# Kernel tuning notes

Measured on AMD Instinct MI355X. Metric: run time of the kernel, lower is better.

Reference implementation:

```python
import jax, jax.numpy as jnp
import numpy as np

N_HEADS = 16


def setup_inputs() -> dict:
    key = jax.random.key(0)
    k0, k1, k2 = jax.random.split(key, 3)
    B, S, D = 8, 1024, 1024
    x = jax.random.normal(k0, (B, S, D), dtype=jnp.float32)
    W_qkv = jax.random.normal(k1, (D, 3 * D), dtype=jnp.float32) * 0.02
    b_qkv = jnp.zeros((3 * D,), dtype=jnp.float32)
    W_proj = jax.random.normal(k2, (D, D), dtype=jnp.float32) * 0.02
    b_proj = jnp.zeros((D,), dtype=jnp.float32)
    return {"x": x, "W_qkv": W_qkv, "b_qkv": b_qkv, "W_proj": W_proj, "b_proj": b_proj}


def reference(x, W_qkv, b_qkv, W_proj, b_proj):
    B, S, D = x.shape
    H = N_HEADS
    hd = D // H
    scale = hd ** (-0.5)
    # qkv projection: (B,S,3D) -> (3,B,H,S,hd)
    qkv = x @ W_qkv + b_qkv
    qkv = qkv.reshape(B, S, 3, H, hd).transpose(2, 0, 3, 1, 4)
    q, k, v = qkv[0], qkv[1], qkv[2]
    # explicit materialized attention scores (B,H,S,S), softmax over keys
    scores = jnp.einsum("bhqd,bhkd->bhqk", q, k) * scale
    attn = jax.nn.softmax(scores, axis=-1)
    # weighted values -> concat heads -> output projection
    out = jnp.einsum("bhqk,bhkd->bhqd", attn, v)
    out = out.transpose(0, 2, 1, 3).reshape(B, S, D)
    return out @ W_proj + b_proj
```

## Files before the change

### kernel.cpp

```cpp
#include <hip/hip_runtime.h>
#include <hip/hip_bf16.h>

typedef __bf16 bf16_t;
typedef __attribute__((ext_vector_type(8))) __bf16 bf16x8;
typedef __attribute__((ext_vector_type(4))) float f32x4;
typedef __attribute__((ext_vector_type(16))) float f32x16;

#define QSCALE 0.18033688011112042f
#define RESCALE_THR 11.5f

#define OFF_XB      ((size_t)0)
#define OFF_WQKVT   ((size_t)16777216)
#define OFF_WPROJT  ((size_t)(16777216 + 6291456))
#define OFF_Q       ((size_t)(16777216 + 6291456 + 2097152))
#define OFF_K       (OFF_Q + (size_t)16777216)
#define OFF_V       (OFF_K + (size_t)16777216)
#define OFF_O       OFF_XB

typedef const __attribute__((address_space(1))) void* as1cv;
typedef __attribute__((address_space(3))) void* as3v;

__device__ __forceinline__ void load_lds16(const void* g, void* l) {
  __builtin_amdgcn_global_load_lds((as1cv)g, (as3v)l, 16, 0, 0);
}

__device__ __forceinline__ f32x4 mfma16(bf16x8 a, bf16x8 b, f32x4 c) {
  return __builtin_amdgcn_mfma_f32_16x16x32_bf16(a, b, c, 0, 0, 0);
}
__device__ __forceinline__ f32x16 mfma32(bf16x8 a, bf16x8 b, f32x16 c) {
  return __builtin_amdgcn_mfma_f32_32x32x16_bf16(a, b, c, 0, 0, 0);
}

__device__ __forceinline__ float fexp2(float x) { return __builtin_amdgcn_exp2f(x); }

__device__ __forceinline__ unsigned pack2bf(float a, float b) {
  union { bf16_t h[2]; unsigned u; } x;
  x.h[0] = (bf16_t)a; x.h[1] = (bf16_t)b;
  return x.u;
}

__device__ __forceinline__ bf16x8 frag_from_words(unsigned w0, unsigned w1,
                                                  unsigned w2, unsigned w3) {
  union { unsigned u[4]; bf16x8 v; } x;
  x.u[0] = w0; x.u[1] = w1; x.u[2] = w2; x.u[3] = w3;
  return x.v;
}

__device__ __forceinline__ bf16x8 ldsr(const bf16_t* lds, int row, int slotbyte) {
  return *(const bf16x8*)((const char*)lds + row * 128 +
                          (slotbyte ^ ((row & 7) << 4)));
}


__global__ __launch_bounds__(256) void cvt_bf16_kernel(
    const float* __restrict__ in, bf16_t* __restrict__ out, int n8) {
  int i = blockIdx.x * blockDim.x + threadIdx.x;
  if (i >= n8) return;
  const float4* p = (const float4*)in + (size_t)i * 2;
  float4 a = p[0], b = p[1];
  bf16x8 o;
  o[0] = (bf16_t)a.x; o[1] = (bf16_t)a.y; o[2] = (bf16_t)a.z; o[3] = (bf16_t)a.w;
  o[4] = (bf16_t)b.x; o[5] = (bf16_t)b.y; o[6] = (bf16_t)b.z; o[7] = (bf16_t)b.w;
  ((bf16x8*)out)[i] = o;
}

__global__ __launch_bounds__(256) void transpose_cvt(
    const float* __restrict__ W, bf16_t* __restrict__ Wt, int rows, int cols) {
  __shared__ float t[32][33];
  const int c0 = blockIdx.x * 32, r0 = blockIdx.y * 32;
  const int tx = threadIdx.x, ty = threadIdx.y;
  for (int rr = ty; rr < 32; rr += 8)
    t[rr][tx] = W[(size_t)(r0 + rr) * cols + c0 + tx];
  __syncthreads();
  for (int rr = ty; rr < 32; rr += 8)
    Wt[(size_t)(c0 + rr) * rows + r0 + tx] = (bf16_t)t[tx][rr];
}


__device__ __forceinline__ void gemm_mainloop_1024(
    const bf16_t* __restrict__ A, const bf16_t* __restrict__ Bt,
    int m0, int n0, bf16_t* Alds, bf16_t* Blds, f32x4 acc[4][4]) {
  const int tid = threadIdx.x;
  const int w = tid >> 6, lane = tid & 63;
  const int wr = w >> 1, wc = w & 1;
  const int lr = lane & 15, lg = lane >> 4;
#pragma unroll
  for (int m = 0; m < 4; ++m)
#pragma unroll
    for (int n = 0; n < 4; ++n)
      acc[m][n] = f32x4{0.f, 0.f, 0.f, 0.f};

  const int crow = lane >> 3;
  const int cels = (((lane & 7) ^ crow) * 8);
  const int rx = (lr & 7) << 4;

  for (int kt = 0; kt < 16; ++kt) {
    const int k0 = kt * 64;
#pragma unroll
    for (int it = 0; it < 4; ++it) {
      const int c = it * 4 + w;
      const int rA = c * 8 + crow;
      load_lds16(A + (size_t)(m0 + rA) * 1024 + k0 + cels, (char*)Alds + c * 1024);
      load_lds16(Bt + (size_t)(n0 + rA) * 1024 + k0 + cels, (char*)Blds + c * 1024);
    }
    asm volatile("s_waitcnt vmcnt(0)" ::: "memory");
    __syncthreads();

    bf16x8 af[4][2], bfr[4][2];
#pragma unroll
    for (int m = 0; m < 4; ++m)
#pragma unroll
      for (int kk = 0; kk < 2; ++kk)
        af[m][kk] = *(const bf16x8*)((const char*)Alds + (wr * 64 + m * 16 + lr) * 128 +
                                     ((kk * 64 + lg * 16) ^ rx));
#pragma unroll
    for (int n = 0; n < 4; ++n)
#pragma unroll
      for (int kk = 0; kk < 2; ++kk)
        bfr[n][kk] = *(const bf16x8*)((const char*)Blds + (wc * 64 + n * 16 + lr) * 128 +
                                      ((kk * 64 + lg * 16) ^ rx));
#pragma unroll
    for (int kk = 0; kk < 2; ++kk)
#pragma unroll
      for (int m = 0; m < 4; ++m)
#pragma unroll
        for (int n = 0; n < 4; ++n)
          acc[m][n] = mfma16(af[m][kk], bfr[n][kk], acc[m][n]);
    __syncthreads();
  }
}

__device__ __forceinline__ void xcd_remap(int bid, int MT_PER, int* mt, int* nt) {
  const int r = bid & 7, q = bid >> 3;
  *mt = r * MT_PER + (q & (MT_PER - 1));
  *nt = q / MT_PER;
}


__global__ __launch_bounds__(256) void gemm_qkv(
    const bf16_t* __restrict__ A, const bf16_t* __restrict__ Bt,
    const float* __restrict__ bias,
    bf16_t* __restrict__ Qh, bf16_t* __restrict__ Kh, bf16_t* __restrict__ Vt) {
  __shared__ alignas(128) bf16_t Alds[128 * 64];
  __shared__ alignas(128) bf16_t Blds[128 * 64];
  int mt, nt;
  xcd_remap(blockIdx.x, 8, &mt, &nt);
  const int m0 = mt * 128, n0 = nt * 128;
  f32x4 acc[4][4];
  gemm_mainloop_1024(A, Bt, m0, n0, Alds, Blds, acc);

  const int tid = threadIdx.x, w = tid >> 6, lane = tid & 63;
  const int wr = w >> 1, wc = w & 1, lr = lane & 15, lg = lane >> 4;
  const int section = n0 >> 10;
#pragma unroll
  for (int n = 0; n < 4; ++n) {
    const int c = n0 + wc * 64 + n * 16 + lr;
    const float bi = bias[c];
    const int d1024 = c & 1023;
    const int h = d1024 >> 6, d = d1024 & 63;
#pragma unroll
    for (int m = 0; m < 4; ++m) {
#pragma unroll
      for (int j = 0; j < 4; ++j) {
        const int r = m0 + wr * 64 + m * 16 + lg * 4 + j;
        const int b = r >> 10, s = r & 1023;
        const size_t hb = ((size_t)(b * 16 + h)) << 16;
        const float v = acc[m][n][j] + bi;
        if (section == 0)      Qh[hb + (size_t)s * 64 + d] = (bf16_t)(v * QSCALE);
        else if (section == 1) Kh[hb + (size_t)s * 64 + d] = (bf16_t)v;
        else                   Vt[hb + (size_t)d * 1024 + s] = (bf16_t)v;
      }
    }
  }
}


__global__ __launch_bounds__(256) void gemm_out(
    const bf16_t* __restrict__ A, const bf16_t* __restrict__ Bt,
    const float* __restrict__ bias, float* __restrict__ out) {
  __shared__ alignas(128) bf16_t Alds[128 * 64];
  __shared__ alignas(128) bf16_t Blds[128 * 64];
  int mt, nt;
  xcd_remap(blockIdx.x, 8, &mt, &nt);
  const int m0 = mt * 128, n0 = nt * 128;
  f32x4 acc[4][4];
  gemm_mainloop_1024(A, Bt, m0, n0, Alds, Blds, acc);

  const int tid = threadIdx.x, w = tid >> 6, lane = tid & 63;
  const int wr = w >> 1, wc = w & 1, lr = lane & 15, lg = lane >> 4;
#pragma unroll
  for (int n = 0; n < 4; ++n) {
    const int c = n0 + wc * 64 + n * 16 + lr;
    const float bi = bias[c];
#pragma unroll
    for (int m = 0; m < 4; ++m)
#pragma unroll
      for (int j = 0; j < 4; ++j) {
        const int r = m0 + wr * 64 + m * 16 + lg * 4 + j;
        out[(size_t)r * 1024 + c] = acc[m][n][j] + bi;
      }
  }
}


__global__ __launch_bounds__(256, 4) void attn_kernel(
    const bf16_t* __restrict__ Qh, const bf16_t* __restrict__ Kh,
    const bf16_t* __restrict__ Vt, bf16_t* __restrict__ Ob) {
  __shared__ alignas(128) bf16_t Klds[2][64 * 64];
  __shared__ alignas(128) bf16_t Vlds[2][64 * 64];

  const int x = blockIdx.x;
  const int bh = ((x & 7) << 4) | (x >> 6);
  const int qt = (x >> 3) & 7;
  const int b = bh >> 4, h = bh & 15;
  const int tid = threadIdx.x, w = tid >> 6, lane = tid & 63;
  const int q31 = lane & 31, hi = lane >> 5;
  const size_t base = (size_t)bh << 16;

  const int qrow0 = qt * 128 + w * 32;

  bf16x8 qf[4];
#pragma unroll
  for (int c = 0; c < 4; ++c)
    qf[c] = *(const bf16x8*)(Qh + base + (size_t)(qrow0 + q31) * 64 + hi * 8 + 16 * c);

  f32x16 oacc0, oacc1;
#pragma unroll
  for (int r = 0; r < 16; ++r) { oacc0[r] = 0.f; oacc1[r] = 0.f; }
  float mreg = -1e30f, lreg = 0.f;

  const int srow = lane >> 3;
  const int sslot = (((lane & 7) ^ srow) << 3);

#define STAGE_KV(bsel, kt_)                                                        \
  do {                                                                             \
    _Pragma("unroll")                                                              \
    for (int it = 0; it < 2; ++it) {                                               \
      const int c = it * 4 + w;                                                    \
      const int r = c * 8 + srow;                                                  \
      load_lds16(Kh + base + (size_t)((kt_) * 64 + r) * 64 + sslot,                \
                 (char*)&Klds[bsel][0] + c * 1024);                                \
      load_lds16(Vt + base + (size_t)r * 1024 + (kt_) * 64 + sslot,                \
                 (char*)&Vlds[bsel][0] + c * 1024);                                \
    }                                                                              \
  } while (0)

  STAGE_KV(0, 0);
  asm volatile("s_waitcnt vmcnt(0)" ::: "memory");
  __syncthreads();
  int cur = 0;

  for (int kt = 0; kt < 16; ++kt) {
    if (kt + 1 < 16) STAGE_KV(cur ^ 1, kt + 1);

    const bf16_t* Kb = &Klds[cur][0];
    const bf16_t* Vb = &Vlds[cur][0];

    f32x16 st0, st1;
#pragma unroll
    for (int r = 0; r < 16; ++r) { st0[r] = 0.f; st1[r] = 0.f; }
#pragma unroll
    for (int c = 0; c < 4; ++c) {
      const int sb = hi * 16 + 32 * c;
      bf16x8 k0 = ldsr(Kb, q31, sb);
      bf16x8 k1 = ldsr(Kb, 32 + q31, sb);
      __builtin_amdgcn_s_setprio(1);
      st0 = mfma32(k0, qf[c], st0);
      st1 = mfma32(k1, qf[c], st1);
      __builtin_amdgcn_s_setprio(0);
    }

    float mx[8];
#pragma unroll
    for (int r = 0; r < 8; ++r)
      mx[r] = fmaxf(fmaxf(st0[r], st0[r + 8]), fmaxf(st1[r], st1[r + 8]));
#pragma unroll
    for (int r = 0; r < 4; ++r) mx[r] = fmaxf(mx[r], mx[r + 4]);
    float tm = fmaxf(fmaxf(mx[0], mx[1]), fmaxf(mx[2], mx[3]));
    tm = fmaxf(tm, __shfl_xor(tm, 32));

    if (!__all(tm - mreg <= RESCALE_THR)) {
      const float mnew = fmaxf(mreg, tm);
      const float corr = fexp2(mreg - mnew);
      lreg *= corr;
#pragma unroll
      for (int r = 0; r < 16; ++r) { oacc0[r] *= corr; oacc1[r] *= corr; }
      mreg = mnew;
    }

    bf16x8 pa[4];
    float psum = 0.f;
#define GROUP(KC, STV, BASE)                                                   \
    {                                                                          \
      const float e0 = fexp2(STV[BASE + 0] - mreg);                            \
      const float e1 = fexp2(STV[BASE + 1] - mreg);                            \
      const float e2 = fexp2(STV[BASE + 2] - mreg);                            \
      const float e3 = fexp2(STV[BASE + 3] - mreg);                            \
      const float e4 = fexp2(STV[BASE + 4] - mreg);                            \
      const float e5 = fexp2(STV[BASE + 5] - mreg);                            \
      const float e6 = fexp2(STV[BASE + 6] - mreg);                            \
      const float e7 = fexp2(STV[BASE + 7] - mreg);                            \
      psum += ((e0 + e1) + (e2 + e3)) + ((e4 + e5) + (e6 + e7));               \
      unsigned wa = pack2bf(e0, e1), wb = pack2bf(e4, e5);                     \
      asm volatile("v_permlane32_swap_b32 %0, %1" : "+v"(wa), "+v"(wb));       \
      unsigned wc = pack2bf(e2, e3), wd = pack2bf(e6, e7);                     \
      asm volatile("v_permlane32_swap_b32 %0, %1" : "+v"(wc), "+v"(wd));       \
      pa[KC] = frag_from_words(wa, wc, wb, wd);                                \
    }
    GROUP(0, st0, 0)
    GROUP(1, st0, 8)
    GROUP(2, st1, 0)
    GROUP(3, st1, 8)
#undef GROUP
    lreg += psum + __shfl_xor(psum, 32);

#pragma unroll
    for (int kc = 0; kc < 4; ++kc) {
      const int sb = hi * 16 + 32 * kc;
      bf16x8 v0 = ldsr(Vb, q31, sb);
      bf16x8 v1 = ldsr(Vb, 32 + q31, sb);
      __builtin_amdgcn_s_setprio(1);
      oacc0 = mfma32(v0, pa[kc], oacc0);
      oacc1 = mfma32(v1, pa[kc], oacc1);
      __builtin_amdgcn_s_setprio(0);
    }

    asm volatile("s_waitcnt vmcnt(0)" ::: "memory");
    __syncthreads();
    cur ^= 1;
  }
#undef STAGE_KV

  const float inv = 1.0f / lreg;
  const int s_tok = qrow0 + q31;
  bf16_t* obase = Ob + (size_t)(b * 1024 + s_tok) * 1024 + h * 64;
#pragma unroll
  for (int i = 0; i < 8; ++i) {
    const int dbase = ((2 * i) & 3) + 8 * ((2 * i) >> 2) + 4 * hi;
    *(unsigned*)(obase + dbase) =
        pack2bf(oacc0[2 * i] * inv, oacc0[2 * i + 1] * inv);
    *(unsigned*)(obase + 32 + dbase) =
        pack2bf(oacc1[2 * i] * inv, oacc1[2 * i + 1] * inv);
  }
}


extern "C" void kernel_launch(void* const* d_in, const int* in_sizes, int n_in,
                              void* d_out, int out_size, void* d_ws, size_t ws_size,
                              hipStream_t stream) {
  const float* x     = (const float*)d_in[0];
  const float* Wqkv  = (const float*)d_in[1];
  const float* bqkv  = (const float*)d_in[2];
  const float* Wproj = (const float*)d_in[3];
  const float* bproj = (const float*)d_in[4];
  float* out = (float*)d_out;
  char* ws = (char*)d_ws;

  bf16_t* Xb  = (bf16_t*)(ws + OFF_XB);
  bf16_t* Wqt = (bf16_t*)(ws + OFF_WQKVT);
  bf16_t* Wpt = (bf16_t*)(ws + OFF_WPROJT);
  bf16_t* Qh  = (bf16_t*)(ws + OFF_Q);
  bf16_t* Kh  = (bf16_t*)(ws + OFF_K);
  bf16_t* Vt  = (bf16_t*)(ws + OFF_V);
  bf16_t* Ob  = (bf16_t*)(ws + OFF_O);

  cvt_bf16_kernel<<<4096, 256, 0, stream>>>(x, Xb, 1048576);
  transpose_cvt<<<dim3(96, 32), dim3(32, 8), 0, stream>>>(Wqkv, Wqt, 1024, 3072);
  transpose_cvt<<<dim3(32, 32), dim3(32, 8), 0, stream>>>(Wproj, Wpt, 1024, 1024);
  gemm_qkv<<<1536, 256, 0, stream>>>(Xb, Wqt, bqkv, Qh, Kh, Vt);
  attn_kernel<<<1024, 256, 0, stream>>>(Qh, Kh, Vt, Ob);
  gemm_out<<<512, 256, 0, stream>>>(Ob, Wpt, bproj, out);
}
```

Measured before the change: 179.4 us.

## Rewrite QKV GEMM with 256x256 tiles, 8 waves and double-buffered LDS pipeline

Replaces the 128x128 QKV projection GEMM with a 512-thread, 256x256-tile kernel. It double-buffers A and B in LDS and interleaves global-to-LDS staging of the next K slice with MFMA phases, using raw s_barrier and s_setprio. The larger tile raises arithmetic intensity and cuts the block count from 1536 to 384. In exchange it uses 128KB of LDS and many more accumulator registers, so occupancy is lower, and it relies on hand-placed waitcnt and barrier ordering for correctness.

```diff
diff --git a/kernel.cpp b/kernel.cpp
--- a/kernel.cpp
+++ b/kernel.cpp
@@ -46,7 +46,7 @@
   return x.v;
 }
 
-__device__ __forceinline__ bf16x8 ldsr(const bf16_t* lds, int row, int slotbyte) {
+__device__ __forceinline__ bf16x8 ldsr(const void* lds, int row, int slotbyte) {
   return *(const bf16x8*)((const char*)lds + row * 128 +
                           (slotbyte ^ ((row & 7) << 4)));
 }
@@ -76,6 +76,153 @@
     Wt[(size_t)(c0 + rr) * rows + r0 + tx] = (bf16_t)t[tx][rr];
 }
 
+#define GBAR asm volatile("s_barrier" ::: "memory")
+
+
+__global__ __launch_bounds__(512, 2) void gemm_qkv(
+    const bf16_t* __restrict__ A, const bf16_t* __restrict__ Bt,
+    const float* __restrict__ bias,
+    bf16_t* __restrict__ Qh, bf16_t* __restrict__ Kh, bf16_t* __restrict__ Vt) {
+  __shared__ alignas(128) char Alds[2 * 32768];
+  __shared__ alignas(128) char Blds[2 * 32768];
+
+  const int rx8 = blockIdx.x & 7, q = blockIdx.x >> 3;
+  const int mt = rx8 * 4 + (q & 3), nt = q >> 2;
+  const int m0 = mt * 256, n0 = nt * 256;
+
+  const int tid = threadIdx.x;
+  const int w = tid >> 6, lane = tid & 63;
+  const int wr = w >> 2, wc = w & 3;
+  const int lr = lane & 15, lg = lane >> 4;
+
+  f32x4 acc[8][4];
+#pragma unroll
+  for (int m = 0; m < 8; ++m)
+#pragma unroll
+    for (int n = 0; n < 4; ++n)
+      acc[m][n] = f32x4{0.f, 0.f, 0.f, 0.f};
+
+  const int srow = tid >> 3;
+  const int scol = (((tid & 7) ^ (srow & 7)) * 8);
+  const int sdst = srow * 128 + ((tid & 7) << 4);
+
+#define STAGE_A_H(b_, kt_, h_) do {                                            \
+    _Pragma("unroll")                                                          \
+    for (int it = 0; it < 2; ++it) {                                           \
+      const int ck = (h_) * 2 + it;                                            \
+      load_lds16(A + (size_t)(m0 + ck * 64 + srow) * 1024 + (kt_) * 64 + scol, \
+                 Alds + (b_) * 32768 + ck * 8192 + sdst);                      \
+    }                                                                          \
+  } while (0)
+#define STAGE_B_H(b_, kt_, h_) do {                                            \
+    _Pragma("unroll")                                                          \
+    for (int it = 0; it < 2; ++it) {                                           \
+      const int ck = (h_) * 2 + it;                                            \
+      load_lds16(Bt + (size_t)(n0 + ck * 64 + srow) * 1024 + (kt_) * 64 + scol,\
+                 Blds + (b_) * 32768 + ck * 8192 + sdst);                      \
+    }                                                                          \
+  } while (0)
+
+  STAGE_B_H(0, 0, 0); STAGE_B_H(0, 0, 1);
+  STAGE_A_H(0, 0, 0); STAGE_A_H(0, 0, 1);
+  asm volatile("s_waitcnt vmcnt(0)" ::: "memory");
+  GBAR;
+
+  const int kb = lg << 4;
+  int cur = 0;
+  for (int s = 0; s < 16; ++s) {
+    const char* Ab = Alds + cur * 32768;
+    const char* Bb = Blds + cur * 32768;
+    const int nxt = cur ^ 1;
+    bf16x8 b0[4], b1[4], af[4];
+
+#pragma unroll
+    for (int n = 0; n < 4; ++n) b0[n] = ldsr(Bb, wc * 64 + n * 16 + lr, kb);
+#pragma unroll
+    for (int m = 0; m < 4; ++m) af[m] = ldsr(Ab, wr * 128 + m * 16 + lr, kb);
+    if (s < 15) { STAGE_B_H(nxt, s + 1, 0); STAGE_B_H(nxt, s + 1, 1); }
+    GBAR;
+    asm volatile("s_waitcnt lgkmcnt(0)" ::: "memory");
+    __builtin_amdgcn_s_setprio(1);
+#pragma unroll
+    for (int m = 0; m < 4; ++m)
+#pragma unroll
+      for (int n = 0; n < 4; ++n)
+        acc[m][n] = mfma16(af[m], b0[n], acc[m][n]);
+    __builtin_amdgcn_s_setprio(0);
+    GBAR;
+
+#pragma unroll
+    for (int n = 0; n < 4; ++n) b1[n] = ldsr(Bb, wc * 64 + n * 16 + lr, 64 + kb);
+#pragma unroll
+    for (int m = 0; m < 4; ++m) af[m] = ldsr(Ab, wr * 128 + m * 16 + lr, 64 + kb);
+    if (s < 15) { STAGE_A_H(nxt, s + 1, 0); STAGE_A_H(nxt, s + 1, 1); }
+    GBAR;
+    asm volatile("s_waitcnt lgkmcnt(0)" ::: "memory");
+    __builtin_amdgcn_s_setprio(1);
+#pragma unroll
+    for (int m = 0; m < 4; ++m)
+#pragma unroll
+      for (int n = 0; n < 4; ++n)
+        acc[m][n] = mfma16(af[m], b1[n], acc[m][n]);
+    __builtin_amdgcn_s_setprio(0);
+    GBAR;
+
+#pragma unroll
+    for (int m = 0; m < 4; ++m) af[m] = ldsr(Ab, wr * 128 + 64 + m * 16 + lr, kb);
+    GBAR;
+    asm volatile("s_waitcnt lgkmcnt(0)" ::: "memory");
+    __builtin_amdgcn_s_setprio(1);
+#pragma unroll
+    for (int m = 0; m < 4; ++m)
+#pragma unroll
+      for (int n = 0; n < 4; ++n)
+        acc[m + 4][n] = mfma16(af[m], b0[n], acc[m + 4][n]);
+    __builtin_amdgcn_s_setprio(0);
+    GBAR;
+
+#pragma unroll
+    for (int m = 0; m < 4; ++m) af[m] = ldsr(Ab, wr * 128 + 64 + m * 16 + lr, 64 + kb);
+    GBAR;
+    asm volatile("s_waitcnt lgkmcnt(0)" ::: "memory");
+    __builtin_amdgcn_s_setprio(1);
+#pragma unroll
+    for (int m = 0; m < 4; ++m)
+#pragma unroll
+      for (int n = 0; n < 4; ++n)
+        acc[m + 4][n] = mfma16(af[m], b1[n], acc[m + 4][n]);
+    __builtin_amdgcn_s_setprio(0);
+    asm volatile("s_waitcnt vmcnt(0)" ::: "memory");
+    GBAR;
+
+    cur ^= 1;
+  }
+#undef STAGE_A_H
+#undef STAGE_B_H
+
+  const int section = n0 >> 10;
+#pragma unroll
+  for (int n = 0; n < 4; ++n) {
+    const int c = n0 + wc * 64 + n * 16 + lr;
+    const float bi = bias[c];
+    const int d1024 = c & 1023;
+    const int h = d1024 >> 6, d = d1024 & 63;
+#pragma unroll
+    for (int m = 0; m < 8; ++m) {
+#pragma unroll
+      for (int j = 0; j < 4; ++j) {
+        const int r = m0 + wr * 128 + m * 16 + lg * 4 + j;
+        const int b = r >> 10, s = r & 1023;
+        const size_t hb = ((size_t)(b * 16 + h)) << 16;
+        const float v = acc[m][n][j] + bi;
+        if (section == 0)      Qh[hb + (size_t)s * 64 + d] = (bf16_t)(v * QSCALE);
+        else if (section == 1) Kh[hb + (size_t)s * 64 + d] = (bf16_t)v;
+        else                   Vt[hb + (size_t)d * 1024 + s] = (bf16_t)v;
+      }
+    }
+  }
+}
+
 
 __device__ __forceinline__ void gemm_mainloop_1024(
     const bf16_t* __restrict__ A, const bf16_t* __restrict__ Bt,
@@ -134,44 +281,6 @@
   const int r = bid & 7, q = bid >> 3;
   *mt = r * MT_PER + (q & (MT_PER - 1));
   *nt = q / MT_PER;
-}
-
-
-__global__ __launch_bounds__(256) void gemm_qkv(
-    const bf16_t* __restrict__ A, const bf16_t* __restrict__ Bt,
-    const float* __restrict__ bias,
-    bf16_t* __restrict__ Qh, bf16_t* __restrict__ Kh, bf16_t* __restrict__ Vt) {
-  __shared__ alignas(128) bf16_t Alds[128 * 64];
-  __shared__ alignas(128) bf16_t Blds[128 * 64];
-  int mt, nt;
-  xcd_remap(blockIdx.x, 8, &mt, &nt);
-  const int m0 = mt * 128, n0 = nt * 128;
-  f32x4 acc[4][4];
-  gemm_mainloop_1024(A, Bt, m0, n0, Alds, Blds, acc);
-
-  const int tid = threadIdx.x, w = tid >> 6, lane = tid & 63;
-  const int wr = w >> 1, wc = w & 1, lr = lane & 15, lg = lane >> 4;
-  const int section = n0 >> 10;
-#pragma unroll
-  for (int n = 0; n < 4; ++n) {
-    const int c = n0 + wc * 64 + n * 16 + lr;
-    const float bi = bias[c];
-    const int d1024 = c & 1023;
-    const int h = d1024 >> 6, d = d1024 & 63;
-#pragma unroll
-    for (int m = 0; m < 4; ++m) {
-#pragma unroll
-      for (int j = 0; j < 4; ++j) {
-        const int r = m0 + wr * 64 + m * 16 + lg * 4 + j;
-        const int b = r >> 10, s = r & 1023;
-        const size_t hb = ((size_t)(b * 16 + h)) << 16;
-        const float v = acc[m][n][j] + bi;
-        if (section == 0)      Qh[hb + (size_t)s * 64 + d] = (bf16_t)(v * QSCALE);
-        else if (section == 1) Kh[hb + (size_t)s * 64 + d] = (bf16_t)v;
-        else                   Vt[hb + (size_t)d * 1024 + s] = (bf16_t)v;
-      }
-    }
-  }
 }
 
 
@@ -367,7 +476,7 @@
   cvt_bf16_kernel<<<4096, 256, 0, stream>>>(x, Xb, 1048576);
   transpose_cvt<<<dim3(96, 32), dim3(32, 8), 0, stream>>>(Wqkv, Wqt, 1024, 3072);
   transpose_cvt<<<dim3(32, 32), dim3(32, 8), 0, stream>>>(Wproj, Wpt, 1024, 1024);
-  gemm_qkv<<<1536, 256, 0, stream>>>(Xb, Wqt, bqkv, Qh, Kh, Vt);
+  gemm_qkv<<<384, 512, 0, stream>>>(Xb, Wqt, bqkv, Qh, Kh, Vt);
   attn_kernel<<<1024, 256, 0, stream>>>(Qh, Kh, Vt, Ob);
   gemm_out<<<512, 256, 0, stream>>>(Ob, Wpt, bproj, out);
 }
```

Result: slower. 197.7 us (+10.2%).
